# Performance work log

Hardware: AMD Instinct MI355X
Metric: run time of the kernel (lower is better)

Reference implementation:

```python
import jax, jax.numpy as jnp
import numpy as np

# Static tree structure: B jets, each a perfect binary tree of depth DEPTH.
B = 64
DEPTH = 12                       # levels 0..DEPTH; level j has B*2**j nodes
N_FEAT = 7
N_HID = 128
LEVEL_SIZES = [B * (1 << j) for j in range(DEPTH + 1)]
OFFSETS = np.concatenate([[0], np.cumsum(LEVEL_SIZES)]).astype(np.int64).tolist()
TOTAL = OFFSETS[-1]              # 524224 nodes
INNER_SIZES = LEVEL_SIZES[:-1]   # all nodes inner except leaf level
INNER_OFF = np.concatenate([[0], np.cumsum(INNER_SIZES)]).astype(np.int64).tolist()


def setup_inputs() -> dict:
    key = jax.random.key(0)
    k_c, k_wu, k_wh = jax.random.split(key, 3)
    contents = jax.random.normal(k_c, (TOTAL, N_FEAT), dtype=jnp.float32)
    # children: per level j < DEPTH, a random pairing (permutation) of level j+1 nodes
    rng = np.random.default_rng(0)
    ch = []
    for j in range(DEPTH):
        perm = rng.permutation(LEVEL_SIZES[j + 1]).astype(np.int32)
        ch.append(perm.reshape(LEVEL_SIZES[j], 2))
    children = jnp.asarray(np.concatenate(ch, axis=0))  # [262080, 2]
    # Learned params (torch nn.Linear: y = x @ W.T + b)
    w_u = jax.random.normal(k_wu, (N_HID, N_FEAT), dtype=jnp.float32) / np.float32(np.sqrt(N_FEAT))
    b_u = jnp.zeros((N_HID,), jnp.float32)
    w_h = jax.random.normal(k_wh, (N_HID, 3 * N_HID), dtype=jnp.float32) / np.float32(np.sqrt(3 * N_HID))
    b_h = jnp.zeros((N_HID,), jnp.float32)
    return {"contents": contents, "children": children,
            "w_u": w_u, "b_u": b_u, "w_h": w_h, "b_h": b_h}


def reference(contents, children, w_u, b_u, w_h, b_h):
    # Bottom-up pass over tree levels (leaves -> root), mirroring the torch loop
    # over levels[::-1]. Perfect binary tree: every non-leaf node is inner.
    emb = None
    for j in range(DEPTH, -1, -1):
        c_j = contents[OFFSETS[j]:OFFSETS[j + 1]]              # [B*2^j, F]
        u = jnp.tanh(c_j @ w_u.T + b_u)                        # [B*2^j, H]
        if j < DEPTH:
            ch_j = children[INNER_OFF[j]:INNER_OFF[j + 1]]     # [B*2^j, 2]
            h_L = emb[ch_j[:, 0]]                              # gather from prev level
            h_R = emb[ch_j[:, 1]]
            emb = jnp.tanh(jnp.concatenate([h_L, h_R, u], axis=1) @ w_h.T + b_h)
        else:
            emb = u  # leaf level: no inner nodes
    return emb.reshape(B, -1)  # root embedding per jet: [B, N_HID]
```

## Files before the change

### kernel.cpp

```cpp
#include <hip/hip_runtime.h>
#include <hip/hip_bf16.h>


#define NF 7
#define NH 128
#define XSTR 136
#define XSTR3 392

typedef __bf16 bf16;
typedef __bf16 bf16x8 __attribute__((ext_vector_type(8)));
typedef float floatx16 __attribute__((ext_vector_type(16)));

__device__ __forceinline__ float ftanh(float x){
    float e = __expf(2.0f * x);
    return 1.0f - __fdividef(2.0f, e + 1.0f);
}

__global__ __launch_bounds__(256) void k_prep(
    const float* __restrict__ contents, const int2* __restrict__ children,
    const float* __restrict__ w_u, const float* __restrict__ b_u,
    const float* __restrict__ w_h,
    unsigned int* __restrict__ usm_u32, int* __restrict__ ids_A,
    int* __restrict__ ids_B, bf16* __restrict__ wb, bf16* __restrict__ w_ub)
{
    __shared__ float csL[128 * 8];
    const int t = threadIdx.x;
    const int b = blockIdx.x;

    if (b >= 512){
        if (b == 512){
            if (t < 64){
                int root = t;
                int* base = ids_B + root * 32;
                const int2* ch0 = children;
                const int2* ch1 = children + 64;
                const int2* ch2 = children + 192;
                const int2* ch3 = children + 448;
                int l1[2], l2[4], l3[8];
                { int2 c = ch0[root]; l1[0] = c.x; l1[1] = c.y; }
                #pragma unroll
                for (int k = 0; k < 2; ++k){ int2 c = ch1[l1[k]]; l2[2*k] = c.x; l2[2*k+1] = c.y; }
                #pragma unroll
                for (int k = 0; k < 4; ++k){ int2 c = ch2[l2[k]]; l3[2*k] = c.x; l3[2*k+1] = c.y; }
                base[0] = root;
                base[1] = l1[0]; base[2] = l1[1];
                #pragma unroll
                for (int k = 0; k < 4; ++k) base[3 + k] = l2[k];
                #pragma unroll
                for (int k = 0; k < 8; ++k) base[7 + k] = l3[k];
                #pragma unroll
                for (int k = 0; k < 8; ++k){
                    int2 c = ch3[l3[k]];
                    base[15 + 2*k] = c.x; base[16 + 2*k] = c.y;
                }
            } else if (t < 192){
                int col = t - 64;
                union { uint4 u4[2]; bf16 h[16]; } row;
                #pragma unroll
                for (int f = 0; f < NF; ++f) row.h[f] = (bf16)w_u[col * NF + f];
                row.h[7] = (bf16)b_u[col];
                #pragma unroll
                for (int k = 8; k < 16; ++k) row.h[k] = (bf16)0.0f;
                *(uint4*)&w_ub[col * 16]     = row.u4[0];
                *(uint4*)&w_ub[col * 16 + 8] = row.u4[1];
            }
        } else if (b < 517){
            int root = (b - 513) * 256 + t;
            int* base = ids_A + root * 128;
            const int2* ch4 = children + 960;
            const int2* ch5 = children + 1984;
            const int2* ch6 = children + 4032;
            const int2* ch7 = children + 8128;
            const int2* ch8 = children + 16320;
            const int2* ch9 = children + 32704;
            int l5[2], l6[4], l7[8], l8[16], l9[32];
            { int2 c = ch4[root]; l5[0] = c.x; l5[1] = c.y; }
            #pragma unroll
            for (int k = 0; k < 2; ++k){ int2 c = ch5[l5[k]]; l6[2*k] = c.x; l6[2*k+1] = c.y; }
            #pragma unroll
            for (int k = 0; k < 4; ++k){ int2 c = ch6[l6[k]]; l7[2*k] = c.x; l7[2*k+1] = c.y; }
            #pragma unroll
            for (int k = 0; k < 8; ++k){ int2 c = ch7[l7[k]]; l8[2*k] = c.x; l8[2*k+1] = c.y; }
            #pragma unroll
            for (int k = 0; k < 16; ++k){ int2 c = ch8[l8[k]]; l9[2*k] = c.x; l9[2*k+1] = c.y; }
            base[0] = root;
            base[1] = l5[0]; base[2] = l5[1];
            #pragma unroll
            for (int k = 0; k < 4; ++k)  base[3 + k]  = l6[k];
            #pragma unroll
            for (int k = 0; k < 8; ++k)  base[7 + k]  = l7[k];
            #pragma unroll
            for (int k = 0; k < 16; ++k) base[15 + k] = l8[k];
            #pragma unroll
            for (int k = 0; k < 32; ++k) base[31 + k] = l9[k];
            #pragma unroll
            for (int k = 0; k < 32; ++k){
                int2 c = ch9[l9[k]];
                base[63 + 2*k] = c.x; base[64 + 2*k] = c.y;
            }
        } else {
            int idx = (b - 517) * 256 + t;
            wb[idx] = (bf16)w_h[idx];
        }
        return;
    }

    const size_t srow = (size_t)b * 128;
    if (t < 224){
        float4 v = ((const float4*)(contents + srow * NF))[t];
        int e = t * 4;
        float vv[4] = {v.x, v.y, v.z, v.w};
        #pragma unroll
        for (int r = 0; r < 4; ++r){ int ee = e + r; csL[(ee/7)*8 + (ee%7)] = vv[r]; }
    }
    const int cp = t & 63;
    const int quarter = t >> 6;
    float wu0[NF], wu1[NF];
    const float* w0 = w_u + (size_t)(2 * cp) * NF;
    #pragma unroll
    for (int f = 0; f < NF; ++f){ wu0[f] = w0[f]; wu1[f] = w0[NF + f]; }
    const float bu0 = b_u[2 * cp], bu1 = b_u[2 * cp + 1];
    __syncthreads();
    #pragma unroll 4
    for (int i = 0; i < 32; ++i){
        int node = quarter * 32 + i;
        float4 c0 = *(const float4*)&csL[node * 8];
        float4 c1 = *(const float4*)&csL[node * 8 + 4];
        float a0 = bu0, a1 = bu1;
        a0 = fmaf(c0.x, wu0[0], a0); a1 = fmaf(c0.x, wu1[0], a1);
        a0 = fmaf(c0.y, wu0[1], a0); a1 = fmaf(c0.y, wu1[1], a1);
        a0 = fmaf(c0.z, wu0[2], a0); a1 = fmaf(c0.z, wu1[2], a1);
        a0 = fmaf(c0.w, wu0[3], a0); a1 = fmaf(c0.w, wu1[3], a1);
        a0 = fmaf(c1.x, wu0[4], a0); a1 = fmaf(c1.x, wu1[4], a1);
        a0 = fmaf(c1.y, wu0[5], a0); a1 = fmaf(c1.y, wu1[5], a1);
        a0 = fmaf(c1.z, wu0[6], a0); a1 = fmaf(c1.z, wu1[6], a1);
        union { unsigned int u; bf16 h[2]; } pk;
        pk.h[0] = (bf16)ftanh(a0);
        pk.h[1] = (bf16)ftanh(a1);
        usm_u32[(srow + node) * 64 + cp] = pk.u;
    }
}

__global__ __launch_bounds__(256, 2) void k_lvl11(
    const float* __restrict__ contents, const int2* __restrict__ children,
    const bf16* __restrict__ w_ub, const bf16* __restrict__ wb,
    const float* __restrict__ b_h, bf16* __restrict__ emb11)
{
    __shared__ bf16 xs[64 * XSTR3];
    __shared__ bf16 ca[192 * 16];
    __shared__ int chS[128];
    const int t = threadIdx.x;
    const int node0 = blockIdx.x * 64;
    const int2* ch11 = children + 131008;
    const float* cont11 = contents + (size_t)131008 * NF;
    const float* contL  = contents + (size_t)262080 * NF;

    if (t < 64){ int2 c = ch11[node0 + t]; chS[2*t] = c.x; chS[2*t + 1] = c.y; }
    __syncthreads();

    if (t < 192){
        const float* src = (t < 128) ? (contL + (size_t)chS[t] * NF)
                                     : (cont11 + (size_t)(node0 + t - 128) * NF);
        union { uint4 u4[2]; bf16 h[16]; } row;
        #pragma unroll
        for (int f = 0; f < NF; ++f) row.h[f] = (bf16)src[f];
        row.h[7] = (bf16)1.0f;
        #pragma unroll
        for (int k = 8; k < 16; ++k) row.h[k] = (bf16)0.0f;
        *(uint4*)&ca[t * 16]     = row.u4[0];
        *(uint4*)&ca[t * 16 + 8] = row.u4[1];
    }

    const int lane = t & 63;
    const int ct = t >> 6;
    const int m = lane & 31;
    const int q = lane >> 5;
    const int colg = ct * 32 + m;
    const bf16x8 bu = *(const bf16x8*)(w_ub + (size_t)colg * 16 + q * 8);
    __syncthreads();

    #pragma unroll
    for (int tile = 0; tile < 6; ++tile){
        bf16x8 a = *(const bf16x8*)&ca[(tile * 32 + m) * 16 + q * 8];
        floatx16 acc = {0,0,0,0,0,0,0,0,0,0,0,0,0,0,0,0};
        acc = __builtin_amdgcn_mfma_f32_32x32x16_bf16(a, bu, acc, 0, 0, 0);
        #pragma unroll
        for (int r = 0; r < 16; ++r){
            int row = (r & 3) + 8 * (r >> 2) + 4 * q;
            bf16 hv = (bf16)ftanh(acc[r]);
            if (tile < 4){
                int c = tile * 32 + row;
                xs[(c >> 1) * XSTR3 + (c & 1) * 128 + colg] = hv;
            } else {
                int i = (tile - 4) * 32 + row;
                xs[i * XSTR3 + 256 + colg] = hv;
            }
        }
    }
    __syncthreads();

    floatx16 acc0 = {0,0,0,0,0,0,0,0,0,0,0,0,0,0,0,0};
    floatx16 acc1 = {0,0,0,0,0,0,0,0,0,0,0,0,0,0,0,0};
    const bf16* bq = wb + (size_t)colg * 384 + q * 8;
    const bf16* xa = &xs[m * XSTR3 + q * 8];
    #pragma unroll
    for (int grp = 0; grp < 3; ++grp){
        bf16x8 bfr[8];
        #pragma unroll
        for (int kk = 0; kk < 8; ++kk)
            bfr[kk] = *(const bf16x8*)(bq + grp * 128 + kk * 16);
        #pragma unroll
        for (int kk = 0; kk < 8; ++kk){
            bf16x8 a0 = *(const bf16x8*)(xa + grp * 128 + kk * 16);
            bf16x8 a1 = *(const bf16x8*)(xa + grp * 128 + kk * 16 + 32 * XSTR3);
            acc0 = __builtin_amdgcn_mfma_f32_32x32x16_bf16(a0, bfr[kk], acc0, 0, 0, 0);
            acc1 = __builtin_amdgcn_mfma_f32_32x32x16_bf16(a1, bfr[kk], acc1, 0, 0, 0);
        }
    }

    const float bv = b_h[colg];
    #pragma unroll
    for (int nt = 0; nt < 2; ++nt){
        const floatx16* accp = nt ? &acc1 : &acc0;
        #pragma unroll
        for (int r = 0; r < 16; ++r){
            int row  = (r & 3) + 8 * (r >> 2) + 4 * q;
            int node = node0 + nt * 32 + row;
            emb11[(size_t)node * NH + colg] = (bf16)ftanh((*accp)[r] + bv);
        }
    }
}

__global__ __launch_bounds__(256, 4) void k_inner(
    const int2* __restrict__ children, const float* __restrict__ contents,
    const float* __restrict__ w_u, const float* __restrict__ b_u,
    const bf16* __restrict__ wb, const float* __restrict__ b_h,
    const bf16* __restrict__ emb_next, bf16* __restrict__ out_b)
{
    __shared__ bf16 xs[64 * XSTR];
    __shared__ int2 ch_s[64];
    __shared__ float cs[64 * 8];
    const int t = threadIdx.x;
    const int block0 = blockIdx.x * 64;
    if (t < 64) ch_s[t] = children[block0 + t];
    if (t < 112){
        float4 v = ((const float4*)(contents + (size_t)block0 * NF))[t];
        int e = t * 4;
        float vv[4] = {v.x, v.y, v.z, v.w};
        #pragma unroll
        for (int r = 0; r < 4; ++r){ int ee = e + r; cs[(ee/7)*8 + (ee%7)] = vv[r]; }
    }
    const int cp = t & 63;
    const int quarter = t >> 6;
    float wu0[NF], wu1[NF];
    {
        const float* w0 = w_u + (size_t)(2 * cp) * NF;
        #pragma unroll
        for (int f = 0; f < NF; ++f){ wu0[f] = w0[f]; wu1[f] = w0[NF + f]; }
    }
    const float bu0 = b_u[2 * cp], bu1 = b_u[2 * cp + 1];
    const int lane = t & 63;
    const int ct = t >> 6;
    const int m = lane & 31;
    const int q = lane >> 5;
    floatx16 acc0 = {0,0,0,0,0,0,0,0,0,0,0,0,0,0,0,0};
    floatx16 acc1 = {0,0,0,0,0,0,0,0,0,0,0,0,0,0,0,0};
    const bf16* bq = wb + ((size_t)(ct * 32 + m) * 384 + q * 8);
    #pragma unroll 1
    for (int p = 0; p < 3; ++p){
        __syncthreads();
        if (p < 2){
            #pragma unroll
            for (int r = 0; r < 4; ++r){
                int task = r * 256 + t;
                int i = task >> 4, part = task & 15;
                int row = (p == 0) ? ch_s[i].x : ch_s[i].y;
                uint4 v = *(const uint4*)(emb_next + (size_t)row * NH + part * 8);
                *(uint4*)&xs[i * XSTR + part * 8] = v;
            }
        } else {
            #pragma unroll 4
            for (int i = 0; i < 16; ++i){
                int node = quarter * 16 + i;
                float4 c0 = *(const float4*)&cs[node * 8];
                float4 c1 = *(const float4*)&cs[node * 8 + 4];
                float a0 = bu0, a1 = bu1;
                a0 = fmaf(c0.x, wu0[0], a0); a1 = fmaf(c0.x, wu1[0], a1);
                a0 = fmaf(c0.y, wu0[1], a0); a1 = fmaf(c0.y, wu1[1], a1);
                a0 = fmaf(c0.z, wu0[2], a0); a1 = fmaf(c0.z, wu1[2], a1);
                a0 = fmaf(c0.w, wu0[3], a0); a1 = fmaf(c0.w, wu1[3], a1);
                a0 = fmaf(c1.x, wu0[4], a0); a1 = fmaf(c1.x, wu1[4], a1);
                a0 = fmaf(c1.y, wu0[5], a0); a1 = fmaf(c1.y, wu1[5], a1);
                a0 = fmaf(c1.z, wu0[6], a0); a1 = fmaf(c1.z, wu1[6], a1);
                union { unsigned int u; bf16 h[2]; } pk;
                pk.h[0] = (bf16)ftanh(a0);
                pk.h[1] = (bf16)ftanh(a1);
                ((unsigned int*)xs)[node * (XSTR / 2) + cp] = pk.u;
            }
        }
        bf16x8 bfr[8];
        #pragma unroll
        for (int kk = 0; kk < 8; ++kk)
            bfr[kk] = *(const bf16x8*)(bq + p * 128 + kk * 16);
        __syncthreads();
        const bf16* xa = &xs[m * XSTR + q * 8];
        #pragma unroll
        for (int kk = 0; kk < 8; ++kk){
            bf16x8 a0 = *(const bf16x8*)(xa + kk * 16);
            bf16x8 a1 = *(const bf16x8*)(xa + kk * 16 + 32 * XSTR);
            acc0 = __builtin_amdgcn_mfma_f32_32x32x16_bf16(a0, bfr[kk], acc0, 0, 0, 0);
            acc1 = __builtin_amdgcn_mfma_f32_32x32x16_bf16(a1, bfr[kk], acc1, 0, 0, 0);
        }
    }
    const int colg = ct * 32 + m;
    const float bv = b_h[colg];
    #pragma unroll
    for (int nt = 0; nt < 2; ++nt){
        const floatx16* accp = nt ? &acc1 : &acc0;
        #pragma unroll
        for (int r = 0; r < 16; ++r){
            int row  = (r & 3) + 8 * (r >> 2) + 4 * q;
            int node = block0 + nt * 32 + row;
            out_b[(size_t)node * NH + colg] = (bf16)ftanh((*accp)[r] + bv);
        }
    }
}

__global__ __launch_bounds__(256, 2) void k_tailA(
    const int* __restrict__ ids_A, const bf16* __restrict__ u_small,
    const bf16* __restrict__ wb, const float* __restrict__ b_h,
    const bf16* __restrict__ emb10, bf16* __restrict__ emb4)
{
    __shared__ bf16 xs[32 * XSTR3];
    __shared__ bf16 embL[32 * 136];
    __shared__ int ids[128];
    const int t = threadIdx.x, root = blockIdx.x;
    const int ct = t >> 6, lane = t & 63, m = lane & 31, q = lane >> 5;
    const float bv = b_h[ct * 32 + m];
    if (t < 32) ((uint4*)ids)[t] = ((const uint4*)(ids_A + root * 128))[t];
    __syncthreads();
    const bf16* bq = wb + ((size_t)(ct * 32 + m) * 384 + q * 8);

    #pragma unroll 1
    for (int l = 9; l >= 4; --l){
        const int n = 1 << (l - 4);
        #pragma unroll 1
        for (int r = 0; r < 4; ++r){
            int task = r * 256 + t;
            if (task < n * 32){
                int i = task >> 5, half = (task >> 4) & 1, part = task & 15;
                uint4 v;
                if (l == 9) v = *(const uint4*)(emb10 + (size_t)ids[63 + 2*i + half] * NH + part * 8);
                else        v = *(uint4*)&embL[(2*i + half) * 136 + part * 8];
                *(uint4*)&xs[i * XSTR3 + half * 128 + part * 8] = v;
            }
        }
        #pragma unroll 1
        for (int r = 0; r < 2; ++r){
            int task = r * 256 + t;
            if (task < n * 16){
                int i = task >> 4, part = task & 15;
                size_t row = (size_t)64 * ((1u << l) - 1) + ids[(n - 1) + i];
                *(uint4*)&xs[i * XSTR3 + 256 + part * 8] =
                    *(const uint4*)(u_small + row * NH + part * 8);
            }
        }
        __syncthreads();
        floatx16 accs[3];
        #pragma unroll
        for (int g = 0; g < 3; ++g) accs[g] = (floatx16){0,0,0,0,0,0,0,0,0,0,0,0,0,0,0,0};
        const bf16* xa = &xs[m * XSTR3 + q * 8];
        #pragma unroll
        for (int grp = 0; grp < 3; ++grp){
            bf16x8 bfr[8];
            #pragma unroll
            for (int kk = 0; kk < 8; ++kk)
                bfr[kk] = *(const bf16x8*)(bq + grp * 128 + kk * 16);
            #pragma unroll
            for (int kk = 0; kk < 8; ++kk){
                bf16x8 a0 = *(const bf16x8*)(xa + grp * 128 + kk * 16);
                accs[grp] = __builtin_amdgcn_mfma_f32_32x32x16_bf16(a0, bfr[kk], accs[grp], 0, 0, 0);
            }
        }
        floatx16 acc = accs[0] + accs[1] + accs[2];
        __syncthreads();
        #pragma unroll
        for (int r = 0; r < 16; ++r){
            int row = (r & 3) + 8 * (r >> 2) + 4 * q;
            if (row < n){
                float v = ftanh(acc[r] + bv);
                if (l > 4) embL[row * 136 + ct * 32 + m] = (bf16)v;
                else       emb4[(size_t)root * NH + ct * 32 + m] = (bf16)v;
            }
        }
        __syncthreads();
    }
}

__global__ __launch_bounds__(256, 2) void k_tailB(
    const int* __restrict__ ids_B, const bf16* __restrict__ u_small,
    const bf16* __restrict__ wb, const float* __restrict__ b_h,
    const bf16* __restrict__ emb4, float* __restrict__ out_f)
{
    __shared__ bf16 xs[8 * XSTR3];
    __shared__ bf16 embL[8 * 136];
    __shared__ int ids[32];
    const int t = threadIdx.x, root = blockIdx.x;
    const int ct = t >> 6, lane = t & 63, m = lane & 31, q = lane >> 5;
    const float bv = b_h[ct * 32 + m];
    if (t < 8) ((uint4*)ids)[t] = ((const uint4*)(ids_B + root * 32))[t];
    __syncthreads();
    const bf16* bq = wb + ((size_t)(ct * 32 + m) * 384 + q * 8);

    #pragma unroll 1
    for (int l = 3; l >= 0; --l){
        const int n = 1 << l;
        {
            int task = t;
            if (task < n * 32){
                int i = task >> 5, half = (task >> 4) & 1, part = task & 15;
                uint4 v;
                if (l == 3) v = *(const uint4*)(emb4 + (size_t)ids[15 + 2*i + half] * NH + part * 8);
                else        v = *(uint4*)&embL[(2*i + half) * 136 + part * 8];
                *(uint4*)&xs[i * XSTR3 + half * 128 + part * 8] = v;
            }
            if (task < n * 16){
                int i = task >> 4, part = task & 15;
                size_t row = (size_t)64 * ((1u << l) - 1) + ids[(n - 1) + i];
                *(uint4*)&xs[i * XSTR3 + 256 + part * 8] =
                    *(const uint4*)(u_small + row * NH + part * 8);
            }
        }
        __syncthreads();
        floatx16 accs[3];
        #pragma unroll
        for (int g = 0; g < 3; ++g) accs[g] = (floatx16){0,0,0,0,0,0,0,0,0,0,0,0,0,0,0,0};
        const bf16* xa = &xs[m * XSTR3 + q * 8];
        #pragma unroll
        for (int grp = 0; grp < 3; ++grp){
            bf16x8 bfr[8];
            #pragma unroll
            for (int kk = 0; kk < 8; ++kk)
                bfr[kk] = *(const bf16x8*)(bq + grp * 128 + kk * 16);
            #pragma unroll
            for (int kk = 0; kk < 8; ++kk){
                bf16x8 a0 = *(const bf16x8*)(xa + grp * 128 + kk * 16);
                accs[grp] = __builtin_amdgcn_mfma_f32_32x32x16_bf16(a0, bfr[kk], accs[grp], 0, 0, 0);
            }
        }
        floatx16 acc = accs[0] + accs[1] + accs[2];
        __syncthreads();
        #pragma unroll
        for (int r = 0; r < 16; ++r){
            int row = (r & 3) + 8 * (r >> 2) + 4 * q;
            if (row < n){
                float v = ftanh(acc[r] + bv);
                if (l > 0) embL[row * 136 + ct * 32 + m] = (bf16)v;
                else       out_f[(size_t)root * NH + ct * 32 + m] = v;
            }
        }
        __syncthreads();
    }
}

extern "C" void kernel_launch(void* const* d_in, const int* in_sizes, int n_in,
                              void* d_out, int out_size, void* d_ws, size_t ws_size,
                              hipStream_t stream){
    const float* contents = (const float*)d_in[0];
    const int2*  children = (const int2*)d_in[1];
    const float* w_u      = (const float*)d_in[2];
    const float* b_u      = (const float*)d_in[3];
    const float* w_h      = (const float*)d_in[4];
    const float* b_h      = (const float*)d_in[5];
    float* outf = (float*)d_out;

    bf16* embA    = (bf16*)d_ws;
    bf16* embB    = embA + (size_t)65536 * NH;
    bf16* wb      = embB + (size_t)131072 * NH;
    bf16* u_small = wb + (size_t)NH * 384;
    int*  ids_A   = (int*)(u_small + (size_t)65536 * NH);
    int*  ids_B   = ids_A + 1024 * 128;
    bf16* w_ub    = (bf16*)(ids_B + 64 * 32);

    hipLaunchKernelGGL(k_prep, dim3(709), dim3(256), 0, stream,
                       contents, children, w_u, b_u, w_h,
                       (unsigned int*)u_small, ids_A, ids_B, wb, w_ub);
    hipLaunchKernelGGL(k_lvl11, dim3(2048), dim3(256), 0, stream,
                       contents, children, w_ub, wb, b_h, embB);
    hipLaunchKernelGGL(k_inner, dim3(1024), dim3(256), 0, stream,
                       children + 65472, contents + (size_t)65472 * NF,
                       w_u, b_u, wb, b_h, embB, embA);
    hipLaunchKernelGGL(k_tailA, dim3(1024), dim3(256), 0, stream,
                       ids_A, u_small, wb, b_h, embA, embB);
    hipLaunchKernelGGL(k_tailB, dim3(64), dim3(256), 0, stream,
                       ids_B, u_small, wb, b_h, embB, outf);
}
```

Before: 223.0 us.

## Split prep kernel and fold u_small computation into level-11 kernel

The old prep kernel did two jobs: index and weight conversion, and computing tanh(W_u c) for the upper levels. The index and weight work now runs in a small k_prep0 launch. The u_small work moves into extra blocks of k_lvl11, so those blocks run alongside the level-11 GEMM blocks rather than in a separate big launch. Level 11 also drops the shared ca staging buffer and one barrier: lanes with q==0 load contents directly into MFMA A-registers inside the tile loop. In exchange, global loads now sit inside the MFMA loop, and level 11 depends on k_prep0 for w_ub and wb.

```diff
diff --git a/kernel.cpp b/kernel.cpp
--- a/kernel.cpp
+++ b/kernel.cpp
@@ -16,160 +16,148 @@
     return 1.0f - __fdividef(2.0f, e + 1.0f);
 }
 
-__global__ __launch_bounds__(256) void k_prep(
+__global__ __launch_bounds__(256) void k_prep0(
+    const int2* __restrict__ children,
+    const float* __restrict__ w_u, const float* __restrict__ b_u,
+    const float* __restrict__ w_h,
+    int* __restrict__ ids_A, int* __restrict__ ids_B,
+    bf16* __restrict__ wb, bf16* __restrict__ w_ub)
+{
+    const int t = threadIdx.x;
+    const int b = blockIdx.x;
+    if (b < 4){
+        int root = b * 256 + t;
+        int* base = ids_A + root * 128;
+        const int2* ch4 = children + 960;
+        const int2* ch5 = children + 1984;
+        const int2* ch6 = children + 4032;
+        const int2* ch7 = children + 8128;
+        const int2* ch8 = children + 16320;
+        const int2* ch9 = children + 32704;
+        int l5[2], l6[4], l7[8], l8[16], l9[32];
+        { int2 c = ch4[root]; l5[0] = c.x; l5[1] = c.y; }
+        #pragma unroll
+        for (int k = 0; k < 2; ++k){ int2 c = ch5[l5[k]]; l6[2*k] = c.x; l6[2*k+1] = c.y; }
+        #pragma unroll
+        for (int k = 0; k < 4; ++k){ int2 c = ch6[l6[k]]; l7[2*k] = c.x; l7[2*k+1] = c.y; }
+        #pragma unroll
+        for (int k = 0; k < 8; ++k){ int2 c = ch7[l7[k]]; l8[2*k] = c.x; l8[2*k+1] = c.y; }
+        #pragma unroll
+        for (int k = 0; k < 16; ++k){ int2 c = ch8[l8[k]]; l9[2*k] = c.x; l9[2*k+1] = c.y; }
+        base[0] = root;
+        base[1] = l5[0]; base[2] = l5[1];
+        #pragma unroll
+        for (int k = 0; k < 4; ++k)  base[3 + k]  = l6[k];
+        #pragma unroll
+        for (int k = 0; k < 8; ++k)  base[7 + k]  = l7[k];
+        #pragma unroll
+        for (int k = 0; k < 16; ++k) base[15 + k] = l8[k];
+        #pragma unroll
+        for (int k = 0; k < 32; ++k) base[31 + k] = l9[k];
+        #pragma unroll
+        for (int k = 0; k < 32; ++k){
+            int2 c = ch9[l9[k]];
+            base[63 + 2*k] = c.x; base[64 + 2*k] = c.y;
+        }
+    } else if (b == 4){
+        if (t < 64){
+            int root = t;
+            int* base = ids_B + root * 32;
+            const int2* ch0 = children;
+            const int2* ch1 = children + 64;
+            const int2* ch2 = children + 192;
+            const int2* ch3 = children + 448;
+            int l1[2], l2[4], l3[8];
+            { int2 c = ch0[root]; l1[0] = c.x; l1[1] = c.y; }
+            #pragma unroll
+            for (int k = 0; k < 2; ++k){ int2 c = ch1[l1[k]]; l2[2*k] = c.x; l2[2*k+1] = c.y; }
+            #pragma unroll
+            for (int k = 0; k < 4; ++k){ int2 c = ch2[l2[k]]; l3[2*k] = c.x; l3[2*k+1] = c.y; }
+            base[0] = root;
+            base[1] = l1[0]; base[2] = l1[1];
+            #pragma unroll
+            for (int k = 0; k < 4; ++k) base[3 + k] = l2[k];
+            #pragma unroll
+            for (int k = 0; k < 8; ++k) base[7 + k] = l3[k];
+            #pragma unroll
+            for (int k = 0; k < 8; ++k){
+                int2 c = ch3[l3[k]];
+                base[15 + 2*k] = c.x; base[16 + 2*k] = c.y;
+            }
+        } else if (t < 192){
+            int col = t - 64;
+            union { uint4 u4[2]; bf16 h[16]; } row;
+            #pragma unroll
+            for (int f = 0; f < NF; ++f) row.h[f] = (bf16)w_u[col * NF + f];
+            row.h[7] = (bf16)b_u[col];
+            #pragma unroll
+            for (int k = 8; k < 16; ++k) row.h[k] = (bf16)0.0f;
+            *(uint4*)&w_ub[col * 16]     = row.u4[0];
+            *(uint4*)&w_ub[col * 16 + 8] = row.u4[1];
+        }
+    } else {
+        int idx = (b - 5) * 256 + t;
+        wb[idx] = (bf16)w_h[idx];
+    }
+}
+
+__global__ __launch_bounds__(256, 2) void k_lvl11(
     const float* __restrict__ contents, const int2* __restrict__ children,
     const float* __restrict__ w_u, const float* __restrict__ b_u,
-    const float* __restrict__ w_h,
-    unsigned int* __restrict__ usm_u32, int* __restrict__ ids_A,
-    int* __restrict__ ids_B, bf16* __restrict__ wb, bf16* __restrict__ w_ub)
+    const bf16* __restrict__ w_ub, const bf16* __restrict__ wb,
+    const float* __restrict__ b_h, bf16* __restrict__ emb11,
+    unsigned int* __restrict__ usm_u32)
 {
-    __shared__ float csL[128 * 8];
+    __shared__ bf16 xs[64 * XSTR3];
+    __shared__ int chS[128];
     const int t = threadIdx.x;
     const int b = blockIdx.x;
 
-    if (b >= 512){
-        if (b == 512){
-            if (t < 64){
-                int root = t;
-                int* base = ids_B + root * 32;
-                const int2* ch0 = children;
-                const int2* ch1 = children + 64;
-                const int2* ch2 = children + 192;
-                const int2* ch3 = children + 448;
-                int l1[2], l2[4], l3[8];
-                { int2 c = ch0[root]; l1[0] = c.x; l1[1] = c.y; }
-                #pragma unroll
-                for (int k = 0; k < 2; ++k){ int2 c = ch1[l1[k]]; l2[2*k] = c.x; l2[2*k+1] = c.y; }
-                #pragma unroll
-                for (int k = 0; k < 4; ++k){ int2 c = ch2[l2[k]]; l3[2*k] = c.x; l3[2*k+1] = c.y; }
-                base[0] = root;
-                base[1] = l1[0]; base[2] = l1[1];
-                #pragma unroll
-                for (int k = 0; k < 4; ++k) base[3 + k] = l2[k];
-                #pragma unroll
-                for (int k = 0; k < 8; ++k) base[7 + k] = l3[k];
-                #pragma unroll
-                for (int k = 0; k < 8; ++k){
-                    int2 c = ch3[l3[k]];
-                    base[15 + 2*k] = c.x; base[16 + 2*k] = c.y;
-                }
-            } else if (t < 192){
-                int col = t - 64;
-                union { uint4 u4[2]; bf16 h[16]; } row;
-                #pragma unroll
-                for (int f = 0; f < NF; ++f) row.h[f] = (bf16)w_u[col * NF + f];
-                row.h[7] = (bf16)b_u[col];
-                #pragma unroll
-                for (int k = 8; k < 16; ++k) row.h[k] = (bf16)0.0f;
-                *(uint4*)&w_ub[col * 16]     = row.u4[0];
-                *(uint4*)&w_ub[col * 16 + 8] = row.u4[1];
-            }
-        } else if (b < 517){
-            int root = (b - 513) * 256 + t;
-            int* base = ids_A + root * 128;
-            const int2* ch4 = children + 960;
-            const int2* ch5 = children + 1984;
-            const int2* ch6 = children + 4032;
-            const int2* ch7 = children + 8128;
-            const int2* ch8 = children + 16320;
-            const int2* ch9 = children + 32704;
-            int l5[2], l6[4], l7[8], l8[16], l9[32];
-            { int2 c = ch4[root]; l5[0] = c.x; l5[1] = c.y; }
-            #pragma unroll
-            for (int k = 0; k < 2; ++k){ int2 c = ch5[l5[k]]; l6[2*k] = c.x; l6[2*k+1] = c.y; }
-            #pragma unroll
-            for (int k = 0; k < 4; ++k){ int2 c = ch6[l6[k]]; l7[2*k] = c.x; l7[2*k+1] = c.y; }
-            #pragma unroll
-            for (int k = 0; k < 8; ++k){ int2 c = ch7[l7[k]]; l8[2*k] = c.x; l8[2*k+1] = c.y; }
-            #pragma unroll
-            for (int k = 0; k < 16; ++k){ int2 c = ch8[l8[k]]; l9[2*k] = c.x; l9[2*k+1] = c.y; }
-            base[0] = root;
-            base[1] = l5[0]; base[2] = l5[1];
-            #pragma unroll
-            for (int k = 0; k < 4; ++k)  base[3 + k]  = l6[k];
-            #pragma unroll
-            for (int k = 0; k < 8; ++k)  base[7 + k]  = l7[k];
-            #pragma unroll
-            for (int k = 0; k < 16; ++k) base[15 + k] = l8[k];
-            #pragma unroll
-            for (int k = 0; k < 32; ++k) base[31 + k] = l9[k];
-            #pragma unroll
-            for (int k = 0; k < 32; ++k){
-                int2 c = ch9[l9[k]];
-                base[63 + 2*k] = c.x; base[64 + 2*k] = c.y;
-            }
-        } else {
-            int idx = (b - 517) * 256 + t;
-            wb[idx] = (bf16)w_h[idx];
+    if (b >= 2048){
+        float* csL = (float*)xs;
+        const size_t srow = (size_t)(b - 2048) * 128;
+        if (t < 224){
+            float4 v = ((const float4*)(contents + srow * NF))[t];
+            int e = t * 4;
+            float vv[4] = {v.x, v.y, v.z, v.w};
+            #pragma unroll
+            for (int r = 0; r < 4; ++r){ int ee = e + r; csL[(ee/7)*8 + (ee%7)] = vv[r]; }
+        }
+        const int cp = t & 63;
+        const int quarter = t >> 6;
+        float wu0[NF], wu1[NF];
+        const float* w0 = w_u + (size_t)(2 * cp) * NF;
+        #pragma unroll
+        for (int f = 0; f < NF; ++f){ wu0[f] = w0[f]; wu1[f] = w0[NF + f]; }
+        const float bu0 = b_u[2 * cp], bu1 = b_u[2 * cp + 1];
+        __syncthreads();
+        #pragma unroll 4
+        for (int i = 0; i < 32; ++i){
+            int node = quarter * 32 + i;
+            float4 c0 = *(const float4*)&csL[node * 8];
+            float4 c1 = *(const float4*)&csL[node * 8 + 4];
+            float a0 = bu0, a1 = bu1;
+            a0 = fmaf(c0.x, wu0[0], a0); a1 = fmaf(c0.x, wu1[0], a1);
+            a0 = fmaf(c0.y, wu0[1], a0); a1 = fmaf(c0.y, wu1[1], a1);
+            a0 = fmaf(c0.z, wu0[2], a0); a1 = fmaf(c0.z, wu1[2], a1);
+            a0 = fmaf(c0.w, wu0[3], a0); a1 = fmaf(c0.w, wu1[3], a1);
+            a0 = fmaf(c1.x, wu0[4], a0); a1 = fmaf(c1.x, wu1[4], a1);
+            a0 = fmaf(c1.y, wu0[5], a0); a1 = fmaf(c1.y, wu1[5], a1);
+            a0 = fmaf(c1.z, wu0[6], a0); a1 = fmaf(c1.z, wu1[6], a1);
+            union { unsigned int u; bf16 h[2]; } pk;
+            pk.h[0] = (bf16)ftanh(a0);
+            pk.h[1] = (bf16)ftanh(a1);
+            usm_u32[(srow + node) * 64 + cp] = pk.u;
         }
         return;
     }
 
-    const size_t srow = (size_t)b * 128;
-    if (t < 224){
-        float4 v = ((const float4*)(contents + srow * NF))[t];
-        int e = t * 4;
-        float vv[4] = {v.x, v.y, v.z, v.w};
-        #pragma unroll
-        for (int r = 0; r < 4; ++r){ int ee = e + r; csL[(ee/7)*8 + (ee%7)] = vv[r]; }
-    }
-    const int cp = t & 63;
-    const int quarter = t >> 6;
-    float wu0[NF], wu1[NF];
-    const float* w0 = w_u + (size_t)(2 * cp) * NF;
-    #pragma unroll
-    for (int f = 0; f < NF; ++f){ wu0[f] = w0[f]; wu1[f] = w0[NF + f]; }
-    const float bu0 = b_u[2 * cp], bu1 = b_u[2 * cp + 1];
-    __syncthreads();
-    #pragma unroll 4
-    for (int i = 0; i < 32; ++i){
-        int node = quarter * 32 + i;
-        float4 c0 = *(const float4*)&csL[node * 8];
-        float4 c1 = *(const float4*)&csL[node * 8 + 4];
-        float a0 = bu0, a1 = bu1;
-        a0 = fmaf(c0.x, wu0[0], a0); a1 = fmaf(c0.x, wu1[0], a1);
-        a0 = fmaf(c0.y, wu0[1], a0); a1 = fmaf(c0.y, wu1[1], a1);
-        a0 = fmaf(c0.z, wu0[2], a0); a1 = fmaf(c0.z, wu1[2], a1);
-        a0 = fmaf(c0.w, wu0[3], a0); a1 = fmaf(c0.w, wu1[3], a1);
-        a0 = fmaf(c1.x, wu0[4], a0); a1 = fmaf(c1.x, wu1[4], a1);
-        a0 = fmaf(c1.y, wu0[5], a0); a1 = fmaf(c1.y, wu1[5], a1);
-        a0 = fmaf(c1.z, wu0[6], a0); a1 = fmaf(c1.z, wu1[6], a1);
-        union { unsigned int u; bf16 h[2]; } pk;
-        pk.h[0] = (bf16)ftanh(a0);
-        pk.h[1] = (bf16)ftanh(a1);
-        usm_u32[(srow + node) * 64 + cp] = pk.u;
-    }
-}
-
-__global__ __launch_bounds__(256, 2) void k_lvl11(
-    const float* __restrict__ contents, const int2* __restrict__ children,
-    const bf16* __restrict__ w_ub, const bf16* __restrict__ wb,
-    const float* __restrict__ b_h, bf16* __restrict__ emb11)
-{
-    __shared__ bf16 xs[64 * XSTR3];
-    __shared__ bf16 ca[192 * 16];
-    __shared__ int chS[128];
-    const int t = threadIdx.x;
-    const int node0 = blockIdx.x * 64;
+    const int node0 = b * 64;
     const int2* ch11 = children + 131008;
     const float* cont11 = contents + (size_t)131008 * NF;
     const float* contL  = contents + (size_t)262080 * NF;
 
     if (t < 64){ int2 c = ch11[node0 + t]; chS[2*t] = c.x; chS[2*t + 1] = c.y; }
-    __syncthreads();
-
-    if (t < 192){
-        const float* src = (t < 128) ? (contL + (size_t)chS[t] * NF)
-                                     : (cont11 + (size_t)(node0 + t - 128) * NF);
-        union { uint4 u4[2]; bf16 h[16]; } row;
-        #pragma unroll
-        for (int f = 0; f < NF; ++f) row.h[f] = (bf16)src[f];
-        row.h[7] = (bf16)1.0f;
-        #pragma unroll
-        for (int k = 8; k < 16; ++k) row.h[k] = (bf16)0.0f;
-        *(uint4*)&ca[t * 16]     = row.u4[0];
-        *(uint4*)&ca[t * 16 + 8] = row.u4[1];
-    }
 
     const int lane = t & 63;
     const int ct = t >> 6;
@@ -181,7 +169,22 @@
 
     #pragma unroll
     for (int tile = 0; tile < 6; ++tile){
-        bf16x8 a = *(const bf16x8*)&ca[(tile * 32 + m) * 16 + q * 8];
+        bf16x8 a = {bf16(0.f),bf16(0.f),bf16(0.f),bf16(0.f),
+                    bf16(0.f),bf16(0.f),bf16(0.f),bf16(0.f)};
+        if (q == 0){
+            const float* src;
+            if (tile < 4){
+                int c = tile * 32 + m;
+                src = contL + (size_t)chS[c] * NF;
+            } else {
+                src = cont11 + (size_t)(node0 + (tile - 4) * 32 + m) * NF;
+            }
+            union { bf16x8 v; bf16 h[8]; } u8;
+            #pragma unroll
+            for (int f = 0; f < NF; ++f) u8.h[f] = (bf16)src[f];
+            u8.h[7] = (bf16)1.0f;
+            a = u8.v;
+        }
         floatx16 acc = {0,0,0,0,0,0,0,0,0,0,0,0,0,0,0,0};
         acc = __builtin_amdgcn_mfma_f32_32x32x16_bf16(a, bu, acc, 0, 0, 0);
         #pragma unroll
@@ -482,11 +485,11 @@
     int*  ids_B   = ids_A + 1024 * 128;
     bf16* w_ub    = (bf16*)(ids_B + 64 * 32);
 
-    hipLaunchKernelGGL(k_prep, dim3(709), dim3(256), 0, stream,
-                       contents, children, w_u, b_u, w_h,
-                       (unsigned int*)u_small, ids_A, ids_B, wb, w_ub);
-    hipLaunchKernelGGL(k_lvl11, dim3(2048), dim3(256), 0, stream,
-                       contents, children, w_ub, wb, b_h, embB);
+    hipLaunchKernelGGL(k_prep0, dim3(197), dim3(256), 0, stream,
+                       children, w_u, b_u, w_h, ids_A, ids_B, wb, w_ub);
+    hipLaunchKernelGGL(k_lvl11, dim3(2560), dim3(256), 0, stream,
+                       contents, children, w_u, b_u, w_ub, wb, b_h,
+                       embB, (unsigned int*)u_small);
     hipLaunchKernelGGL(k_inner, dim3(1024), dim3(256), 0, stream,
                        children + 65472, contents + (size_t)65472 * NF,
                        w_u, b_u, wb, b_h, embB, embA);
```

After: 219.2 us. About the same (-1.7%).
